# Kernel optimization log

Hardware: AMD Instinct MI355X
Metric: run time of the kernel (lower is better)

The kernel has to match this reference:

```python
import jax, jax.numpy as jnp
import numpy as np

N_EMBD = 256; N_HEAD = 16; CTX = 2048
V_HD = 32; KV_RANK = 32; Q_RANK = 96
ROPE_HD = 64; NOPE_HD = 32; HEAD_D = ROPE_HD + NOPE_HD  # 96
N_KEEP = CTX // 4  # 512
C_CURV = 1.0
EPS = 1e-6
B, T = 2, 2048


def rmsnorm(x, w):
    return x * jax.lax.rsqrt(jnp.mean(x * x, axis=-1, keepdims=True) + EPS) * w


def logmap(x, u, c):
    # log map from hyperbolic point x toward u (Poincare ball, curvature c)
    xn = jnp.linalg.norm(x, axis=-1, keepdims=True)
    sf = 2.0 / (1.0 + c * xn ** 2)                      # scaling_factor(x, c)
    mx = -x
    un = jnp.linalg.norm(u, axis=-1, keepdims=True)
    ip = jnp.sum(mx * u, axis=-1, keepdims=True)
    num = (1 + 2 * c * ip + c * un ** 2) * mx + (1 - c * xn ** 2) * u
    den = 1 + 2 * c * ip + (c ** 2) * (xn ** 2) * (un ** 2)
    mob = num / den                                      # mobius_addition(-x, u, c)
    an = jnp.linalg.norm(mob, axis=-1, keepdims=True)
    cf = 2.0 / (sf * (c ** 0.5))
    arg = jnp.clip(jnp.sqrt(c) * jnp.sqrt(an), -0.999, 0.999)
    return cf * jnp.arctanh(arg) * (mob / an)


def rope_apply(x, cos_seq, sin_seq):
    # x: [B,H,T,D]; cos/sin: [T,D//2] -> broadcast [1,1,T,D//2]
    c = cos_seq[None, None]; s = sin_seq[None, None]
    xr, xi = jnp.split(x, 2, axis=-1)
    return jnp.concatenate([xr * c - xi * s, xr * s + xi * c], axis=-1)


def attn(q, k, v, causal):
    d = q.shape[-1]
    s = jnp.einsum('bhqd,bhkd->bhqk', q, k) / jnp.sqrt(jnp.asarray(d, q.dtype))
    if causal:
        mask = jnp.tril(jnp.ones((s.shape[-2], s.shape[-1]), bool))
        s = jnp.where(mask, s, -jnp.inf)
    p = jax.nn.softmax(s, axis=-1)
    return jnp.einsum('bhqk,bhkd->bhqd', p, v)


def setup_inputs() -> dict:
    key = jax.random.key(0)
    ks = jax.random.split(key, 20)
    w = lambda k, shp: (jax.random.normal(k, shp, jnp.float32) * 0.02)
    NOPE_DIM = N_HEAD * NOPE_HD   # 512
    ROPE_DIM = N_HEAD * ROPE_HD   # 1024
    VAL_DIM = N_HEAD * V_HD       # 512
    # precompute_freqs_cis(rope_head_dim, ctx_len)
    freqs = 1.0 / (10000.0 ** (np.arange(0, ROPE_HD, 2, dtype=np.float32) / ROPE_HD))
    t = np.arange(CTX, dtype=np.float32)
    ang = np.outer(t, freqs)
    return {
        'x': jax.random.normal(ks[0], (B, T, N_EMBD), jnp.float32),
        'W_cq': w(ks[1], (N_EMBD, Q_RANK)),
        'q_norm_w': jnp.ones((Q_RANK,), jnp.float32),
        'W_dqn': w(ks[2], (Q_RANK, NOPE_DIM)),
        'W_dqr': w(ks[3], (Q_RANK, ROPE_DIM)),
        'W_ckv': w(ks[4], (N_EMBD, KV_RANK)),
        'kv_norm_w': jnp.ones((KV_RANK,), jnp.float32),
        'W_dkn': w(ks[5], (KV_RANK, NOPE_DIM)),
        'W_dv': w(ks[6], (KV_RANK, VAL_DIM)),
        'W_kr': w(ks[7], (N_EMBD, ROPE_HD)),
        'W_imp': w(ks[8], (N_EMBD, 1)),
        'b_imp': jnp.zeros((1,), jnp.float32),
        'W_selk': w(ks[9], (N_EMBD, N_HEAD * HEAD_D)),
        'W_selv': w(ks[10], (N_EMBD, VAL_DIM)),
        'W_wink': w(ks[11], (N_EMBD, N_HEAD * HEAD_D)),
        'W_winv': w(ks[12], (N_EMBD, VAL_DIM)),
        'W_gate': w(ks[13], (N_EMBD, 3)),
        'b_gate': jnp.zeros((3,), jnp.float32),
        'W_proj': w(ks[14], (N_HEAD * V_HD, N_EMBD)),
        'cos_f': jnp.asarray(np.cos(ang)),
        'sin_f': jnp.asarray(np.sin(ang)),
    }


def reference(x, W_cq, q_norm_w, W_dqn, W_dqr, W_ckv, kv_norm_w, W_dkn, W_dv, W_kr,
              W_imp, b_imp, W_selk, W_selv, W_wink, W_winv, W_gate, b_gate, W_proj,
              cos_f, sin_f):
    Bx, Tx, C = x.shape
    ref = jnp.pad(x[:, :-1, :], ((0, 0), (1, 0), (0, 0)))   # calculate_reference_point
    xh = logmap(ref, x, C_CURV)
    # compressed query path
    nq = rmsnorm(xh @ W_cq, q_norm_w)
    qn = (nq @ W_dqn).reshape(Bx, Tx, N_HEAD, NOPE_HD).transpose(0, 2, 1, 3)
    qr = (nq @ W_dqr).reshape(Bx, Tx, N_HEAD, ROPE_HD).transpose(0, 2, 1, 3)
    qr = rope_apply(qr, cos_f[:Tx], sin_f[:Tx])
    q = jnp.concatenate([qn, qr], axis=-1)                  # [B,H,T,96]
    # branch gate
    bw = jax.nn.softmax(jnp.mean(x @ W_gate + b_gate, axis=1), axis=-1)  # [B,3]
    # compressed KV path
    nkv = rmsnorm(x @ W_ckv, kv_norm_w)
    kn = (nkv @ W_dkn).reshape(Bx, Tx, N_HEAD, NOPE_HD).transpose(0, 2, 1, 3)
    v = (nkv @ W_dv).reshape(Bx, Tx, N_HEAD, V_HD).transpose(0, 2, 1, 3)
    kr = rope_apply((x @ W_kr)[:, None], cos_f[:Tx], sin_f[:Tx])  # [B,1,T,64]
    kr = jnp.broadcast_to(kr, (Bx, N_HEAD, Tx, ROPE_HD))
    k = jnp.concatenate([kn, kr], axis=-1)
    out_cmp = attn(q, k, v, causal=True)
    # token-selection branch (top-k important tokens, sorted)
    scores = (x @ W_imp + b_imp)[..., 0]                    # [B,T]
    _, idx = jax.lax.top_k(scores, min(N_KEEP, Tx))
    idx = jnp.sort(idx, axis=1)
    sel = jnp.take_along_axis(x, idx[:, :, None], axis=1)   # [B,K,C]
    sk = (sel @ W_selk).reshape(Bx, -1, N_HEAD, HEAD_D).transpose(0, 2, 1, 3)
    sv = (sel @ W_selv).reshape(Bx, -1, N_HEAD, V_HD).transpose(0, 2, 1, 3)
    out_sel = attn(q, sk, sv, causal=False)
    # sliding-window branch (training path -> full sequence, causal)
    wk = (x @ W_wink).reshape(Bx, Tx, N_HEAD, HEAD_D).transpose(0, 2, 1, 3)
    wv = (x @ W_winv).reshape(Bx, Tx, N_HEAD, V_HD).transpose(0, 2, 1, 3)
    out_win = attn(q, wk, wv, causal=True)
    w3 = bw[:, :, None, None, None]
    out = w3[:, 0] * out_cmp + w3[:, 1] * out_sel + w3[:, 2] * out_win
    out = out.transpose(0, 2, 1, 3).reshape(Bx, Tx, N_HEAD * V_HD)
    return out @ W_proj
```

## Files before the change

kernel.cpp:

```cpp
#include <hip/hip_runtime.h>
#include <hip/hip_bf16.h>
#include <math.h>

#define TT 2048
#define NE 256
#define NHEAD 16

typedef __attribute__((ext_vector_type(8))) short bf16x8;
typedef __attribute__((ext_vector_type(4))) float f32x4;
typedef __attribute__((ext_vector_type(16))) float f32x16;
typedef unsigned short ushort;
typedef __attribute__((ext_vector_type(8))) unsigned short us8;

__device__ __forceinline__ short f2bf(float x) {
  __hip_bfloat16 h = __float2bfloat16(x);
  return *reinterpret_cast<short*>(&h);
}
__device__ __forceinline__ float bf2f(ushort u) {
  unsigned v = ((unsigned)u) << 16;
  return __uint_as_float(v);
}

__global__ __launch_bounds__(256) void logmap_kernel(const float* __restrict__ x,
                                                     ushort* __restrict__ xhb,
                                                     ushort* __restrict__ xbf) {
  __shared__ float red[16];
  int row = blockIdx.x, tid = threadIdx.x;
  int t = row & (TT - 1);
  float uv = x[row * NE + tid];
  float rv = (t == 0) ? 0.f : x[row * NE - NE + tid];
  xbf[row * NE + tid] = (ushort)f2bf(uv);
  float a = rv * rv, bq = uv * uv, c2 = -rv * uv;
#pragma unroll
  for (int off = 32; off > 0; off >>= 1) {
    a += __shfl_down(a, off, 64);
    bq += __shfl_down(bq, off, 64);
    c2 += __shfl_down(c2, off, 64);
  }
  if ((tid & 63) == 0) {
    int w = tid >> 6;
    red[w] = a; red[4 + w] = bq; red[8 + w] = c2;
  }
  __syncthreads();
  float xn2 = red[0] + red[1] + red[2] + red[3];
  float un2 = red[4] + red[5] + red[6] + red[7];
  float ip  = red[8] + red[9] + red[10] + red[11];
  float den = 1.f + 2.f * ip + xn2 * un2;
  float mob = ((1.f + 2.f * ip + un2) * (-rv) + (1.f - xn2) * uv) / den;
  float m2 = mob * mob;
#pragma unroll
  for (int off = 32; off > 0; off >>= 1) m2 += __shfl_down(m2, off, 64);
  if ((tid & 63) == 0) red[12 + (tid >> 6)] = m2;
  __syncthreads();
  float an2 = red[12] + red[13] + red[14] + red[15];
  float an = sqrtf(an2);
  float cf = 1.f + xn2;
  float arg = fminf(sqrtf(an), 0.999f);
  xhb[row * NE + tid] = (ushort)f2bf(cf * atanhf(arg) * mob / an);
}

__global__ __launch_bounds__(256) void wtconv_all_kernel(
    const float* __restrict__ W_dqn, const float* __restrict__ W_dqr,
    const float* __restrict__ W_dkn, const float* __restrict__ W_dv,
    const float* __restrict__ W_selk, const float* __restrict__ W_selv,
    const float* __restrict__ W_wink, const float* __restrict__ W_winv,
    const float* __restrict__ W_proj, const float* __restrict__ W_cq,
    const float* __restrict__ W_ckv, const float* __restrict__ W_kr,
    const float* __restrict__ W_gate, const float* __restrict__ W_imp,
    ushort* __restrict__ Wt_q, ushort* __restrict__ Wt_kv,
    ushort* __restrict__ Wt_sel, ushort* __restrict__ Wt_win,
    ushort* __restrict__ Wt_proj, ushort* __restrict__ Wt_cq,
    ushort* __restrict__ Wt_nkv) {
  int i = blockIdx.x * 256 + threadIdx.x;
  const float scale = 0.147244458176154f;
  if (i < 147456) {
    int k = i / 1536, n = i - k * 1536;
    float v = (n < 512) ? W_dqn[(size_t)k * 512 + n] : W_dqr[(size_t)k * 1024 + (n - 512)];
    Wt_q[(size_t)n * 96 + k] = (ushort)f2bf(v * scale);
  } else if (i < 180224) {
    int j = i - 147456;
    int k = j >> 10, n = j & 1023;
    float v = (n < 512) ? W_dkn[(size_t)k * 512 + n] : W_dv[(size_t)k * 512 + (n - 512)];
    Wt_kv[(size_t)n * 32 + k] = (ushort)f2bf(v);
  } else if (i < 704512) {
    int j = i - 180224;
    int k = j >> 11, n = j & 2047;
    float v = (n < 1536) ? W_selk[(size_t)k * 1536 + n] : W_selv[(size_t)k * 512 + (n - 1536)];
    Wt_sel[(size_t)n * 256 + k] = (ushort)f2bf(v);
  } else if (i < 1228800) {
    int j = i - 704512;
    int k = j >> 11, n = j & 2047;
    float v = (n < 1536) ? W_wink[(size_t)k * 1536 + n] : W_winv[(size_t)k * 512 + (n - 1536)];
    Wt_win[(size_t)n * 256 + k] = (ushort)f2bf(v);
  } else if (i < 1359872) {
    int j = i - 1228800;
    int k = j >> 8, n = j & 255;
    Wt_proj[(size_t)n * 512 + k] = (ushort)f2bf(W_proj[(size_t)k * 256 + n]);
  } else if (i < 1392640) {
    int j = i - 1359872;
    int k = j >> 7, n = j & 127;
    float v = (n < 96) ? W_cq[(size_t)k * 96 + n] : 0.f;
    Wt_cq[(size_t)n * 256 + k] = (ushort)f2bf(v);
  } else if (i < 1425408) {
    int j = i - 1392640;
    int k = j >> 7, n = j & 127;
    float v;
    if (n < 32) v = W_ckv[(size_t)k * 32 + n];
    else if (n < 96) v = W_kr[(size_t)k * 64 + (n - 32)];
    else if (n < 99) v = W_gate[(size_t)k * 3 + (n - 96)];
    else if (n == 99) v = W_imp[k];
    else v = 0.f;
    Wt_nkv[(size_t)n * 256 + k] = (ushort)f2bf(v);
  }
}

__global__ __launch_bounds__(256) void gemm_kernel(const ushort* __restrict__ A,
                                                   const ushort* __restrict__ Bt,
                                                   void* __restrict__ Out,
                                                   const ushort* __restrict__ A2,
                                                   const ushort* __restrict__ Bt2,
                                                   void* __restrict__ Out2,
                                                   const int* __restrict__ selidx,
                                                   const float* __restrict__ cosp,
                                                   const float* __restrict__ sinp,
                                                   int K, int ldo, int obf16, int ropemode) {
  __shared__ __align__(16) short As[128 * 40];
  __shared__ __align__(16) short Bs[128 * 40];
  if (blockIdx.z == 1) { A = A2; Bt = Bt2; Out = Out2; }
  int m0 = blockIdx.x * 128, n0 = blockIdx.y * 128;
  int tid = threadIdx.x;
  int wv = tid >> 6, lane = tid & 63;
  int l15 = lane & 15, quad = lane >> 4;
  int wm = wv >> 1, wn = wv & 1;

  int r = tid >> 1, seg = tid & 1;
  int arow = m0 + r;
  if (selidx) arow = ((arow >> 9) * TT) + selidx[m0 + r];
  const ushort* ga = A + (size_t)arow * K + seg * 16;
  const ushort* gb = Bt + (size_t)(n0 + r) * K + seg * 16;

  f32x4 acc[4][4];
#pragma unroll
  for (int i = 0; i < 4; ++i)
#pragma unroll
    for (int j = 0; j < 4; ++j) acc[i][j] = (f32x4){0.f, 0.f, 0.f, 0.f};

  int nk = K >> 5;
  us8 apre0 = *(const us8*)ga, apre1 = *(const us8*)(ga + 8);
  us8 bpre0 = *(const us8*)gb, bpre1 = *(const us8*)(gb + 8);
  for (int kk = 0; kk < nk; ++kk) {
    __syncthreads();
    *(us8*)(As + r * 40 + seg * 16) = apre0;
    *(us8*)(As + r * 40 + seg * 16 + 8) = apre1;
    *(us8*)(Bs + r * 40 + seg * 16) = bpre0;
    *(us8*)(Bs + r * 40 + seg * 16 + 8) = bpre1;
    __syncthreads();
    if (kk + 1 < nk) {
      apre0 = *(const us8*)(ga + (kk + 1) * 32);
      apre1 = *(const us8*)(ga + (kk + 1) * 32 + 8);
      bpre0 = *(const us8*)(gb + (kk + 1) * 32);
      bpre1 = *(const us8*)(gb + (kk + 1) * 32 + 8);
    }
    bf16x8 af[4], bf[4];
#pragma unroll
    for (int mf = 0; mf < 4; ++mf)
      af[mf] = *(const bf16x8*)(As + (wm * 64 + mf * 16 + l15) * 40 + quad * 8);
#pragma unroll
    for (int nf = 0; nf < 4; ++nf)
      bf[nf] = *(const bf16x8*)(Bs + (wn * 64 + nf * 16 + l15) * 40 + quad * 8);
#pragma unroll
    for (int mf = 0; mf < 4; ++mf)
#pragma unroll
      for (int nf = 0; nf < 4; ++nf)
        acc[mf][nf] = __builtin_amdgcn_mfma_f32_16x16x32_bf16(af[mf], bf[nf], acc[mf][nf], 0, 0, 0);
  }

  if (ropemode && blockIdx.y >= 4) {
#pragma unroll
    for (int mf = 0; mf < 4; ++mf) {
#pragma unroll
      for (int nf = 0; nf < 2; ++nf) {
        int dd = nf * 16 + l15;
#pragma unroll
        for (int reg = 0; reg < 4; ++reg) {
          int row = m0 + wm * 64 + mf * 16 + quad * 4 + reg;
          int t = row & (TT - 1);
          float c = cosp[t * 32 + dd], s = sinp[t * 32 + dd];
          float xr = acc[mf][nf][reg], xi = acc[mf][nf + 2][reg];
          int col = n0 + wn * 64 + nf * 16 + l15;
          size_t oi = (size_t)row * ldo + col;
          ((ushort*)Out)[oi] = (ushort)f2bf(xr * c - xi * s);
          ((ushort*)Out)[oi + 32] = (ushort)f2bf(xr * s + xi * c);
        }
      }
    }
    return;
  }
#pragma unroll
  for (int mf = 0; mf < 4; ++mf) {
#pragma unroll
    for (int nf = 0; nf < 4; ++nf) {
#pragma unroll
      for (int reg = 0; reg < 4; ++reg) {
        int row = m0 + wm * 64 + mf * 16 + quad * 4 + reg;
        int col = n0 + wn * 64 + nf * 16 + l15;
        size_t oi = (size_t)row * ldo + col;
        float v = acc[mf][nf][reg];
        if (obf16) ((ushort*)Out)[oi] = (ushort)f2bf(v);
        else ((float*)Out)[oi] = v;
      }
    }
  }
}

__global__ __launch_bounds__(128) void norm_kernel(const float* __restrict__ nkvraw,
                                                   const float* __restrict__ nqraw,
                                                   const float* __restrict__ x,
                                                   const float* __restrict__ W_imp,
                                                   const float* __restrict__ b_imp,
                                                   const float* __restrict__ kvnw,
                                                   const float* __restrict__ qnw,
                                                   const float* __restrict__ cos_t,
                                                   const float* __restrict__ sin_t,
                                                   ushort* __restrict__ nkvb,
                                                   ushort* __restrict__ krbf,
                                                   float* __restrict__ scores,
                                                   ushort* __restrict__ nqb) {
  int tid = threadIdx.x;
  if (blockIdx.x < 4096) {
    int row = blockIdx.x;
    int t = row & (TT - 1);
    if (tid < 32) {
      float v = nkvraw[(size_t)row * 128 + tid];
      float ss = v * v;
#pragma unroll
      for (int off = 16; off > 0; off >>= 1) ss += __shfl_xor(ss, off, 32);
      nkvb[(size_t)row * 32 + tid] = (ushort)f2bf(v * rsqrtf(ss / 32.f + 1e-6f) * kvnw[tid]);
    } else if (tid < 64) {
      int dd = tid - 32;
      float xr = nkvraw[(size_t)row * 128 + 32 + dd];
      float xi = nkvraw[(size_t)row * 128 + 64 + dd];
      float c = cos_t[t * 32 + dd], s = sin_t[t * 32 + dd];
      krbf[(size_t)row * 64 + dd] = (ushort)f2bf(xr * c - xi * s);
      krbf[(size_t)row * 64 + dd + 32] = (ushort)f2bf(xr * s + xi * c);
    } else {
      int lane = tid - 64;
      float p = 0.f;
#pragma unroll
      for (int k = 0; k < 4; ++k) p += x[(size_t)row * 256 + lane + k * 64] * W_imp[lane + k * 64];
#pragma unroll
      for (int off = 32; off > 0; off >>= 1) p += __shfl_down(p, off, 64);
      if (lane == 0) scores[row] = p + b_imp[0];
    }
  } else {
    int row = blockIdx.x - 4096;
    __shared__ float red2[2];
    float v = (tid < 96) ? nqraw[(size_t)row * 128 + tid] : 0.f;
    float p = v * v;
#pragma unroll
    for (int off = 32; off > 0; off >>= 1) p += __shfl_down(p, off, 64);
    if ((tid & 63) == 0) red2[tid >> 6] = p;
    __syncthreads();
    float ss = red2[0] + red2[1];
    float sc = rsqrtf(ss / 96.f + 1e-6f);
    if (tid < 96) nqb[(size_t)row * 96 + tid] = (ushort)f2bf(v * sc * qnw[tid]);
  }
}

__global__ __launch_bounds__(256) void gate_kernel(const float* __restrict__ nkvraw,
                                                   const float* __restrict__ b_gate,
                                                   float* __restrict__ bw) {
  int tid = threadIdx.x;
  float a0 = 0, a1 = 0, a2 = 0, a3 = 0, a4 = 0, a5 = 0;
  for (int r = tid; r < 2 * TT; r += 256) {
    float g0 = nkvraw[(size_t)r * 128 + 96];
    float g1 = nkvraw[(size_t)r * 128 + 97];
    float g2 = nkvraw[(size_t)r * 128 + 98];
    if (r < TT) { a0 += g0; a1 += g1; a2 += g2; }
    else { a3 += g0; a4 += g1; a5 += g2; }
  }
  __shared__ float red[6][256];
  red[0][tid] = a0; red[1][tid] = a1; red[2][tid] = a2;
  red[3][tid] = a3; red[4][tid] = a4; red[5][tid] = a5;
  __syncthreads();
  for (int s = 128; s > 0; s >>= 1) {
    if (tid < s) {
#pragma unroll
      for (int q = 0; q < 6; ++q) red[q][tid] += red[q][tid + s];
    }
    __syncthreads();
  }
  if (tid == 0) {
    for (int b = 0; b < 2; ++b) {
      float v[3];
      float mx = -INFINITY;
      for (int j = 0; j < 3; ++j) {
        v[j] = red[b * 3 + j][0] / (float)TT + b_gate[j];
        mx = fmaxf(mx, v[j]);
      }
      float sum = 0.f;
      for (int j = 0; j < 3; ++j) { v[j] = expf(v[j] - mx); sum += v[j]; }
      for (int j = 0; j < 3; ++j) bw[b * 3 + j] = v[j] / sum;
    }
  }
}

__global__ __launch_bounds__(1024) void topk_rank_kernel(const float* __restrict__ scores,
                                                         int* __restrict__ flags) {
  int b = blockIdx.y, blk = blockIdx.x;
  int tid = threadIdx.x;
  __shared__ unsigned sk[TT];
#pragma unroll
  for (int e = 0; e < 2; ++e) {
    int i = tid + e * 1024;
    float s = scores[b * TT + i];
    unsigned u = __float_as_uint(s);
    u = (u & 0x80000000u) ? ~u : (u | 0x80000000u);
    sk[i] = u;
  }
  __syncthreads();
  int e = blk * 64 + (tid >> 4);
  int sub = tid & 15;
  unsigned u = sk[e];
  int r = 0;
  int j0 = sub * 128;
#pragma unroll 8
  for (int j = j0; j < j0 + 128; ++j) {
    unsigned v = sk[j];
    r += (int)((v > u) || (v == u && j < e));
  }
#pragma unroll
  for (int off = 8; off > 0; off >>= 1) r += __shfl_down(r, off, 16);
  if (sub == 0) flags[b * TT + e] = (r < 512) ? 1 : 0;
}

__global__ __launch_bounds__(1024) void topk_scan_kernel(const int* __restrict__ flags,
                                                         int* __restrict__ selidx) {
  int b = blockIdx.x, tid = threadIdx.x;
  __shared__ int pre[TT];
  int f0 = flags[b * TT + tid], f1 = flags[b * TT + tid + 1024];
  pre[tid] = f0;
  pre[tid + 1024] = f1;
  __syncthreads();
  for (int off = 1; off < TT; off <<= 1) {
    int a0 = (tid >= off) ? pre[tid - off] : 0;
    int a1 = (tid + 1024 >= off) ? pre[tid + 1024 - off] : 0;
    __syncthreads();
    pre[tid] += a0;
    pre[tid + 1024] += a1;
    __syncthreads();
  }
  if (f0) selidx[b * 512 + pre[tid] - 1] = tid;
  if (f1) selidx[b * 512 + pre[tid + 1024] - 1] = tid + 1024;
}

__global__ __launch_bounds__(512, 4) void flash_fused_kernel(
    const ushort* __restrict__ qbf,
    const ushort* __restrict__ kv,
    const ushort* __restrict__ krbf,
    const ushort* __restrict__ selt,
    const ushort* __restrict__ wint,
    const float* __restrict__ bw,
    ushort* __restrict__ attout) {
  __shared__ __align__(16) short smem[13312 + 4608 + 256];
  short* Ksm = smem;
  short* Vtm = smem + 13312;
  float* Ls  = (float*)(smem + 17920);

  int bx = blockIdx.x;
  int j = bx >> 5;
  int qtile = (j < 8) ? (15 - 2 * j) : (2 * (j - 8));
  int bh = bx & 31;
  int b = bh >> 4, h = bh & 15;
  int tid = threadIdx.x;
  int wv = tid >> 6;
  int qsub = wv >> 1;
  int khalf = wv & 1;
  int lane = tid & 63;
  int l31 = lane & 31, half = lane >> 5;

  int qrow0 = qtile * 128;
  for (int i = tid; i < 128 * 24; i += 512) {
    int qi = i / 24, dp = (i - qi * 24) * 4;
    int col = (dp < 32) ? (h * 32 + dp) : (512 + h * 64 + (dp - 32));
    *(ushort4*)(Ksm + qi * 104 + dp) =
        *(const ushort4*)(qbf + (size_t)(b * TT + qrow0 + qi) * 1536 + col);
  }
  __syncthreads();
  bf16x8 qf[6];
#pragma unroll
  for (int ks = 0; ks < 6; ++ks)
    qf[ks] = *(const bf16x8*)(Ksm + (qsub * 32 + l31) * 104 + ks * 16 + half * 8);
  __syncthreads();

  short* kdst[3];
#pragma unroll
  for (int c = 0; c < 3; ++c) {
    int i = c * 512 + tid;
    int kj = i / 24, dp = (i - kj * 24) * 4;
    kdst[c] = &Ksm[kj * 104 + dp];
  }
  int vd0 = (tid & 15) * 2, vkjp = (tid >> 4) * 2;
  short* vdsta = &Vtm[(vd0 + 0) * 72 + vkjp];
  short* vdstb = &Vtm[(vd0 + 1) * 72 + vkjp];

  f32x16 oacc;
#pragma unroll
  for (int r2 = 0; r2 < 16; ++r2) oacc[r2] = 0.f;

#define PREFETCH(KP, VA, VB)                                  \
  {                                                           \
    _Pragma("unroll") for (int c = 0; c < 3; ++c) {           \
      KP[c] = *(const ushort4*)ksrc[c];                       \
      ksrc[c] += kstep[c];                                    \
    }                                                         \
    VA = *(const ushort2*)vsrcA;                              \
    VB = *(const ushort2*)vsrcB;                              \
    vsrcA += vstep;                                           \
    vsrcB += vstep;                                           \
  }

#define COMMIT(KP, VA, VB, SL)                                           \
  {                                                                      \
    _Pragma("unroll") for (int c = 0; c < 3; ++c)                        \
      *(ushort4*)(kdst[c] + (SL) * (64 * 104)) = KP[c];                  \
    *(unsigned*)(vdsta + (SL) * (32 * 72)) =                             \
        (unsigned)VA.x | ((unsigned)VB.x << 16);                         \
    *(unsigned*)(vdstb + (SL) * (32 * 72)) =                             \
        (unsigned)VA.y | ((unsigned)VB.y << 16);                         \
  }

  for (int s = 0; s < 3; ++s) {
    const ushort *kb1, *kb2, *vb;
    size_t krs1, krs2, vrs;
    int split, Tk, causal;
    if (s == 0) {
      kb1 = kv + h * 32;        krs1 = 1024; split = 32;
      kb2 = krbf;               krs2 = 64;
      vb = kv + 512 + h * 32;   vrs = 1024;
      Tk = TT; causal = 1;
    } else if (s == 1) {
      kb1 = selt + h * 96;      krs1 = 2048; split = 96;
      kb2 = selt;               krs2 = 2048;
      vb = selt + 1536 + h * 32; vrs = 2048;
      Tk = 512; causal = 0;
    } else {
      kb1 = wint + h * 96;      krs1 = 2048; split = 96;
      kb2 = wint;               krs2 = 2048;
      vb = wint + 1536 + h * 32; vrs = 2048;
      Tk = TT; causal = 1;
    }
    size_t bTk = (size_t)b * Tk;

    const ushort* ksrc[3];
    int kstep[3];
#pragma unroll
    for (int c = 0; c < 3; ++c) {
      int i = c * 512 + tid;
      int kj = i / 24, dp = (i - kj * 24) * 4;
      if (dp < split) { ksrc[c] = kb1 + (bTk + kj) * krs1 + dp; kstep[c] = (int)(64 * krs1); }
      else            { ksrc[c] = kb2 + (bTk + kj) * krs2 + (dp - split); kstep[c] = (int)(64 * krs2); }
    }
    const ushort* vsrcA = vb + (bTk + vkjp) * vrs + vd0;
    const ushort* vsrcB = vb + (bTk + vkjp + 1) * vrs + vd0;
    int vstep = (int)(64 * vrs);

    ushort4 kpre0[3], kpre1[3];
    ushort2 vpa0, vpb0, vpa1, vpb1;

    f32x16 of;
#pragma unroll
    for (int r2 = 0; r2 < 16; ++r2) of[r2] = 0.f;
    float lsum = 0.f;

    auto do_tile = [&](int kt, const short* Kss, const short* Vss) {
      int krow0 = kt * 64;
      f32x16 sfT[2];
#pragma unroll
      for (int r2 = 0; r2 < 16; ++r2) { sfT[0][r2] = 0.f; sfT[1][r2] = 0.f; }
#pragma unroll
      for (int ks = 0; ks < 6; ++ks) {
#pragma unroll
        for (int kb = 0; kb < 2; ++kb) {
          bf16x8 ak = *(const bf16x8*)(Kss + (kb * 32 + l31) * 104 + ks * 16 + half * 8);
          sfT[kb] = __builtin_amdgcn_mfma_f32_32x32x16_bf16(ak, qf[ks], sfT[kb], 0, 0, 0);
        }
      }
      int qg = qrow0 + qsub * 32 + l31;
      int domask = causal && (kt >= 2 * qtile);
      unsigned w01[2][4], w23[2][4];
#pragma unroll
      for (int kb = 0; kb < 2; ++kb) {
#pragma unroll
        for (int gg = 0; gg < 4; ++gg) {
          int key0 = krow0 + kb * 32 + 8 * gg + 4 * half;
          float t0 = sfT[kb][gg * 4 + 0];
          float t1 = sfT[kb][gg * 4 + 1];
          float t2 = sfT[kb][gg * 4 + 2];
          float t3 = sfT[kb][gg * 4 + 3];
          if (domask) {
            if (key0 + 0 > qg) t0 = -INFINITY;
            if (key0 + 1 > qg) t1 = -INFINITY;
            if (key0 + 2 > qg) t2 = -INFINITY;
            if (key0 + 3 > qg) t3 = -INFINITY;
          }
          float p0 = __builtin_amdgcn_exp2f(fminf(t0, 43.3f));
          float p1 = __builtin_amdgcn_exp2f(fminf(t1, 43.3f));
          float p2 = __builtin_amdgcn_exp2f(fminf(t2, 43.3f));
          float p3 = __builtin_amdgcn_exp2f(fminf(t3, 43.3f));
          lsum += (p0 + p1) + (p2 + p3);
          asm("v_cvt_pk_bf16_f32 %0, %1, %2" : "=v"(w01[kb][gg]) : "v"(p0), "v"(p1));
          asm("v_cvt_pk_bf16_f32 %0, %1, %2" : "=v"(w23[kb][gg]) : "v"(p2), "v"(p3));
        }
      }
#pragma unroll
      for (int ks2 = 0; ks2 < 4; ++ks2) {
        int kb = ks2 >> 1, gA = 2 * (ks2 & 1);
        unsigned a0 = w01[kb][gA], b0 = w01[kb][gA + 1];
        unsigned a1 = w23[kb][gA], b1 = w23[kb][gA + 1];
        asm("v_permlane32_swap_b32 %0, %1" : "+v"(a0), "+v"(b0));
        asm("v_permlane32_swap_b32 %0, %1" : "+v"(a1), "+v"(b1));
        union { unsigned u[4]; bf16x8 v; } ap;
        ap.u[0] = a0; ap.u[1] = a1; ap.u[2] = b0; ap.u[3] = b1;
        bf16x8 bv = *(const bf16x8*)(Vss + l31 * 72 + ks2 * 16 + half * 8);
        of = __builtin_amdgcn_mfma_f32_32x32x16_bf16(ap.v, bv, of, 0, 0, 0);
      }
    };

    int nkt = causal ? (2 * qtile + 2) : 8;
    PREFETCH(kpre0, vpa0, vpb0);
    PREFETCH(kpre1, vpa1, vpb1);
    for (int kt = 0; kt < nkt; kt += 2) {
      __syncthreads();
      COMMIT(kpre0, vpa0, vpb0, 0);
      COMMIT(kpre1, vpa1, vpb1, 1);
      if (kt + 2 < nkt) PREFETCH(kpre0, vpa0, vpb0);
      if (kt + 3 < nkt) PREFETCH(kpre1, vpa1, vpb1);
      __syncthreads();
      if (khalf == 0) do_tile(kt, Ksm, Vtm);
      else            do_tile(kt + 1, Ksm + 64 * 104, Vtm + 32 * 72);
    }

    lsum += __shfl_xor(lsum, 32, 64);
    __syncthreads();
    float* red = (float*)Ksm;
    int rbase = (qsub * 64 + lane) * 17;
    if (khalf == 1) {
#pragma unroll
      for (int r2 = 0; r2 < 16; ++r2) red[rbase + r2] = of[r2];
      red[rbase + 16] = lsum;
    }
    __syncthreads();
    if (khalf == 0) {
#pragma unroll
      for (int r2 = 0; r2 < 16; ++r2) of[r2] += red[rbase + r2];
      lsum += red[rbase + 16];
      if (half == 0) Ls[qsub * 32 + l31] = lsum;
    }
    asm volatile("s_waitcnt lgkmcnt(0)" ::: "memory");
    if (khalf == 0) {
      float wgt = bw[b * 3 + s];
#pragma unroll
      for (int reg = 0; reg < 16; ++reg) {
        int ql = (reg & 3) + 8 * (reg >> 2) + 4 * half;
        oacc[reg] += of[reg] * (wgt / Ls[qsub * 32 + ql]);
      }
    }
  }
#undef PREFETCH
#undef COMMIT

  if (khalf == 0) {
#pragma unroll
    for (int reg = 0; reg < 16; ++reg) {
      int trow = qrow0 + qsub * 32 + (reg & 3) + 8 * (reg >> 2) + 4 * half;
      attout[(size_t)(b * TT + trow) * 512 + h * 32 + l31] = (ushort)f2bf(oacc[reg]);
    }
  }
}

extern "C" void kernel_launch(void* const* d_in, const int* in_sizes, int n_in,
                              void* d_out, int out_size, void* d_ws, size_t ws_size,
                              hipStream_t stream) {
  const float* x      = (const float*)d_in[0];
  const float* W_cq   = (const float*)d_in[1];
  const float* qnw    = (const float*)d_in[2];
  const float* W_dqn  = (const float*)d_in[3];
  const float* W_dqr  = (const float*)d_in[4];
  const float* W_ckv  = (const float*)d_in[5];
  const float* kvnw   = (const float*)d_in[6];
  const float* W_dkn  = (const float*)d_in[7];
  const float* W_dv   = (const float*)d_in[8];
  const float* W_kr   = (const float*)d_in[9];
  const float* W_imp  = (const float*)d_in[10];
  const float* b_imp  = (const float*)d_in[11];
  const float* W_selk = (const float*)d_in[12];
  const float* W_selv = (const float*)d_in[13];
  const float* W_wink = (const float*)d_in[14];
  const float* W_winv = (const float*)d_in[15];
  const float* W_gate = (const float*)d_in[16];
  const float* b_gate = (const float*)d_in[17];
  const float* W_proj = (const float*)d_in[18];
  const float* cos_f  = (const float*)d_in[19];
  const float* sin_f  = (const float*)d_in[20];
  float* out = (float*)d_out;
  float* ws  = (float*)d_ws;

  size_t off = 0;
  auto alloc = [&](size_t n) {
    float* p = ws + off;
    off += (n + 255) & ~(size_t)255;
    return p;
  };
  const int ROWS = 2 * TT;
  ushort* xbf     = (ushort*)alloc((size_t)ROWS * 128);
  ushort* xhb     = (ushort*)alloc((size_t)ROWS * 128);
  float* nqraw    = alloc((size_t)ROWS * 128);
  float* nkvraw   = alloc((size_t)ROWS * 128);
  ushort* nqb     = (ushort*)alloc((size_t)ROWS * 48);
  ushort* qbf     = (ushort*)alloc((size_t)ROWS * 768);
  ushort* nkvb    = (ushort*)alloc((size_t)ROWS * 16);
  ushort* kvtmp   = (ushort*)alloc((size_t)ROWS * 512);
  ushort* krbf    = (ushort*)alloc((size_t)ROWS * 32);
  float* scores   = alloc(ROWS);
  float* bwp      = alloc(8);
  int* selidx     = (int*)alloc(1024);
  int* selflags   = (int*)alloc(ROWS);
  ushort* seltmp  = (ushort*)alloc((size_t)1024 * 1024);
  ushort* wintmp  = (ushort*)alloc((size_t)ROWS * 1024);
  ushort* attoutb = (ushort*)alloc((size_t)ROWS * 256);
  ushort* Wt_q    = (ushort*)alloc((size_t)1536 * 48);
  ushort* Wt_kv   = (ushort*)alloc((size_t)1024 * 16);
  ushort* Wt_sel  = (ushort*)alloc((size_t)2048 * 128);
  ushort* Wt_win  = (ushort*)alloc((size_t)2048 * 128);
  ushort* Wt_proj = (ushort*)alloc((size_t)256 * 256);
  ushort* Wt_cq   = (ushort*)alloc((size_t)128 * 128);
  ushort* Wt_nkv  = (ushort*)alloc((size_t)128 * 128);

  wtconv_all_kernel<<<5568, 256, 0, stream>>>(
      W_dqn, W_dqr, W_dkn, W_dv, W_selk, W_selv, W_wink, W_winv, W_proj,
      W_cq, W_ckv, W_kr, W_gate, W_imp,
      Wt_q, Wt_kv, Wt_sel, Wt_win, Wt_proj, Wt_cq, Wt_nkv);

  logmap_kernel<<<ROWS, 256, 0, stream>>>(x, xhb, xbf);

  gemm_kernel<<<dim3(32, 1, 2), 256, 0, stream>>>(xhb, Wt_cq, nqraw, xbf, Wt_nkv, nkvraw,
                                                  nullptr, nullptr, nullptr, 256, 128, 0, 0);
  norm_kernel<<<2 * ROWS, 128, 0, stream>>>(nkvraw, nqraw, x, W_imp, b_imp, kvnw, qnw,
                                            cos_f, sin_f, nkvb, krbf, scores, nqb);
  gemm_kernel<<<dim3(32, 12), 256, 0, stream>>>(nqb, Wt_q, qbf, nullptr, nullptr, nullptr,
                                                nullptr, cos_f, sin_f, 96, 1536, 1, 1);
  gemm_kernel<<<dim3(32, 8), 256, 0, stream>>>(nkvb, Wt_kv, kvtmp, nullptr, nullptr, nullptr,
                                               nullptr, nullptr, nullptr, 32, 1024, 1, 0);
  gate_kernel<<<1, 256, 0, stream>>>(nkvraw, b_gate, bwp);
  topk_rank_kernel<<<dim3(32, 2), 1024, 0, stream>>>(scores, selflags);
  topk_scan_kernel<<<2, 1024, 0, stream>>>(selflags, selidx);
  gemm_kernel<<<dim3(8, 16), 256, 0, stream>>>(xbf, Wt_sel, seltmp, nullptr, nullptr, nullptr,
                                               selidx, nullptr, nullptr, 256, 2048, 1, 0);
  gemm_kernel<<<dim3(32, 16), 256, 0, stream>>>(xbf, Wt_win, wintmp, nullptr, nullptr, nullptr,
                                                nullptr, nullptr, nullptr, 256, 2048, 1, 0);

  flash_fused_kernel<<<512, 512, 0, stream>>>(qbf, kvtmp, krbf, seltmp, wintmp, bwp, attoutb);

  gemm_kernel<<<dim3(32, 2), 256, 0, stream>>>(attoutb, Wt_proj, out, nullptr, nullptr, nullptr,
                                               nullptr, nullptr, nullptr, 512, 256, 0, 0);
}
```

Measured before the change: 299.5 us.

## Merge launches: fuse logmap into weight prep, batch GEMMs, fold gate into GEMM epilogue

Merges the logmap and weight-conversion kernels into one prep kernel, and batches independent GEMMs (q/kv projections, window/selection projections) into single launches through a z-dimension with per-slice parameters. The gate reduction moves into the first GEMM's epilogue via atomics, and the gate softmax is computed inside the flash kernel. The top-k scan is rewritten with a wave-shuffle prefix sum, and flash launch bounds change from 4 to 2. The intent is to cut launch overhead and serial small kernels, at the cost of atomics, early-return blocks in the batched GEMMs, and a different occupancy hint for flash.

```diff
diff --git a/kernel.cpp b/kernel.cpp
--- a/kernel.cpp
+++ b/kernel.cpp
@@ -21,45 +21,8 @@
   return __uint_as_float(v);
 }
 
-__global__ __launch_bounds__(256) void logmap_kernel(const float* __restrict__ x,
-                                                     ushort* __restrict__ xhb,
-                                                     ushort* __restrict__ xbf) {
-  __shared__ float red[16];
-  int row = blockIdx.x, tid = threadIdx.x;
-  int t = row & (TT - 1);
-  float uv = x[row * NE + tid];
-  float rv = (t == 0) ? 0.f : x[row * NE - NE + tid];
-  xbf[row * NE + tid] = (ushort)f2bf(uv);
-  float a = rv * rv, bq = uv * uv, c2 = -rv * uv;
-#pragma unroll
-  for (int off = 32; off > 0; off >>= 1) {
-    a += __shfl_down(a, off, 64);
-    bq += __shfl_down(bq, off, 64);
-    c2 += __shfl_down(c2, off, 64);
-  }
-  if ((tid & 63) == 0) {
-    int w = tid >> 6;
-    red[w] = a; red[4 + w] = bq; red[8 + w] = c2;
-  }
-  __syncthreads();
-  float xn2 = red[0] + red[1] + red[2] + red[3];
-  float un2 = red[4] + red[5] + red[6] + red[7];
-  float ip  = red[8] + red[9] + red[10] + red[11];
-  float den = 1.f + 2.f * ip + xn2 * un2;
-  float mob = ((1.f + 2.f * ip + un2) * (-rv) + (1.f - xn2) * uv) / den;
-  float m2 = mob * mob;
-#pragma unroll
-  for (int off = 32; off > 0; off >>= 1) m2 += __shfl_down(m2, off, 64);
-  if ((tid & 63) == 0) red[12 + (tid >> 6)] = m2;
-  __syncthreads();
-  float an2 = red[12] + red[13] + red[14] + red[15];
-  float an = sqrtf(an2);
-  float cf = 1.f + xn2;
-  float arg = fminf(sqrtf(an), 0.999f);
-  xhb[row * NE + tid] = (ushort)f2bf(cf * atanhf(arg) * mob / an);
-}
-
-__global__ __launch_bounds__(256) void wtconv_all_kernel(
+__global__ __launch_bounds__(256) void prep_kernel(
+    const float* __restrict__ x, ushort* __restrict__ xhb, ushort* __restrict__ xbf,
     const float* __restrict__ W_dqn, const float* __restrict__ W_dqr,
     const float* __restrict__ W_dkn, const float* __restrict__ W_dv,
     const float* __restrict__ W_selk, const float* __restrict__ W_selv,
@@ -70,8 +33,45 @@
     ushort* __restrict__ Wt_q, ushort* __restrict__ Wt_kv,
     ushort* __restrict__ Wt_sel, ushort* __restrict__ Wt_win,
     ushort* __restrict__ Wt_proj, ushort* __restrict__ Wt_cq,
-    ushort* __restrict__ Wt_nkv) {
-  int i = blockIdx.x * 256 + threadIdx.x;
+    ushort* __restrict__ Wt_nkv, float* __restrict__ gacc) {
+  __shared__ float red[16];
+  int bx = blockIdx.x, tid = threadIdx.x;
+  if (bx < 4096) {
+    int row = bx;
+    int t = row & (TT - 1);
+    float uv = x[row * NE + tid];
+    float rv = (t == 0) ? 0.f : x[row * NE - NE + tid];
+    xbf[row * NE + tid] = (ushort)f2bf(uv);
+    float a = rv * rv, bq = uv * uv, c2 = -rv * uv;
+#pragma unroll
+    for (int off = 32; off > 0; off >>= 1) {
+      a += __shfl_down(a, off, 64);
+      bq += __shfl_down(bq, off, 64);
+      c2 += __shfl_down(c2, off, 64);
+    }
+    if ((tid & 63) == 0) {
+      int w = tid >> 6;
+      red[w] = a; red[4 + w] = bq; red[8 + w] = c2;
+    }
+    __syncthreads();
+    float xn2 = red[0] + red[1] + red[2] + red[3];
+    float un2 = red[4] + red[5] + red[6] + red[7];
+    float ip  = red[8] + red[9] + red[10] + red[11];
+    float den = 1.f + 2.f * ip + xn2 * un2;
+    float mob = ((1.f + 2.f * ip + un2) * (-rv) + (1.f - xn2) * uv) / den;
+    float m2 = mob * mob;
+#pragma unroll
+    for (int off = 32; off > 0; off >>= 1) m2 += __shfl_down(m2, off, 64);
+    if ((tid & 63) == 0) red[12 + (tid >> 6)] = m2;
+    __syncthreads();
+    float an2 = red[12] + red[13] + red[14] + red[15];
+    float an = sqrtf(an2);
+    float cf = 1.f + xn2;
+    float arg = fminf(sqrtf(an), 0.999f);
+    xhb[row * NE + tid] = (ushort)f2bf(cf * atanhf(arg) * mob / an);
+    return;
+  }
+  int i = (bx - 4096) * 256 + tid;
   const float scale = 0.147244458176154f;
   if (i < 147456) {
     int k = i / 1536, n = i - k * 1536;
@@ -111,6 +111,8 @@
     else if (n == 99) v = W_imp[k];
     else v = 0.f;
     Wt_nkv[(size_t)n * 256 + k] = (ushort)f2bf(v);
+  } else if (i < 1425414) {
+    gacc[i - 1425408] = 0.f;
   }
 }
 
@@ -120,13 +122,21 @@
                                                    const ushort* __restrict__ A2,
                                                    const ushort* __restrict__ Bt2,
                                                    void* __restrict__ Out2,
-                                                   const int* __restrict__ selidx,
+                                                   const int* __restrict__ selidx2,
                                                    const float* __restrict__ cosp,
                                                    const float* __restrict__ sinp,
-                                                   int K, int ldo, int obf16, int ropemode) {
+                                                   float* __restrict__ gateacc,
+                                                   int K, int ldo, int obf16, int ropemode,
+                                                   int K2, int ldo2, int obf2, int rope2,
+                                                   int xlim2, int ylim2) {
   __shared__ __align__(16) short As[128 * 40];
   __shared__ __align__(16) short Bs[128 * 40];
-  if (blockIdx.z == 1) { A = A2; Bt = Bt2; Out = Out2; }
+  const int* selidx = nullptr;
+  if (blockIdx.z == 1) {
+    if ((int)blockIdx.x >= xlim2 || (int)blockIdx.y >= ylim2) return;
+    A = A2; Bt = Bt2; Out = Out2; selidx = selidx2;
+    K = K2; ldo = ldo2; obf16 = obf2; ropemode = rope2;
+  }
   int m0 = blockIdx.x * 128, n0 = blockIdx.y * 128;
   int tid = threadIdx.x;
   int wv = tid >> 6, lane = tid & 63;
@@ -210,6 +220,14 @@
         else ((float*)Out)[oi] = v;
       }
     }
+  }
+  if (gateacc != nullptr && blockIdx.z == 1 && wn == 1 && l15 < 3) {
+    float ssum = 0.f;
+#pragma unroll
+    for (int mf = 0; mf < 4; ++mf)
+#pragma unroll
+      for (int reg = 0; reg < 4; ++reg) ssum += acc[mf][2][reg];
+    atomicAdd(&gateacc[(m0 >> 11) * 3 + l15], ssum);
   }
 }
 
@@ -267,44 +285,6 @@
   }
 }
 
-__global__ __launch_bounds__(256) void gate_kernel(const float* __restrict__ nkvraw,
-                                                   const float* __restrict__ b_gate,
-                                                   float* __restrict__ bw) {
-  int tid = threadIdx.x;
-  float a0 = 0, a1 = 0, a2 = 0, a3 = 0, a4 = 0, a5 = 0;
-  for (int r = tid; r < 2 * TT; r += 256) {
-    float g0 = nkvraw[(size_t)r * 128 + 96];
-    float g1 = nkvraw[(size_t)r * 128 + 97];
-    float g2 = nkvraw[(size_t)r * 128 + 98];
-    if (r < TT) { a0 += g0; a1 += g1; a2 += g2; }
-    else { a3 += g0; a4 += g1; a5 += g2; }
-  }
-  __shared__ float red[6][256];
-  red[0][tid] = a0; red[1][tid] = a1; red[2][tid] = a2;
-  red[3][tid] = a3; red[4][tid] = a4; red[5][tid] = a5;
-  __syncthreads();
-  for (int s = 128; s > 0; s >>= 1) {
-    if (tid < s) {
-#pragma unroll
-      for (int q = 0; q < 6; ++q) red[q][tid] += red[q][tid + s];
-    }
-    __syncthreads();
-  }
-  if (tid == 0) {
-    for (int b = 0; b < 2; ++b) {
-      float v[3];
-      float mx = -INFINITY;
-      for (int j = 0; j < 3; ++j) {
-        v[j] = red[b * 3 + j][0] / (float)TT + b_gate[j];
-        mx = fmaxf(mx, v[j]);
-      }
-      float sum = 0.f;
-      for (int j = 0; j < 3; ++j) { v[j] = expf(v[j] - mx); sum += v[j]; }
-      for (int j = 0; j < 3; ++j) bw[b * 3 + j] = v[j] / sum;
-    }
-  }
-}
-
 __global__ __launch_bounds__(1024) void topk_rank_kernel(const float* __restrict__ scores,
                                                          int* __restrict__ flags) {
   int b = blockIdx.y, blk = blockIdx.x;
@@ -337,30 +317,34 @@
 __global__ __launch_bounds__(1024) void topk_scan_kernel(const int* __restrict__ flags,
                                                          int* __restrict__ selidx) {
   int b = blockIdx.x, tid = threadIdx.x;
-  __shared__ int pre[TT];
-  int f0 = flags[b * TT + tid], f1 = flags[b * TT + tid + 1024];
-  pre[tid] = f0;
-  pre[tid + 1024] = f1;
+  __shared__ int wsum[16];
+  int2 f = *(const int2*)(flags + b * TT + 2 * tid);
+  int local = f.x + f.y;
+  int lane = tid & 63, wv = tid >> 6;
+  int sc = local;
+#pragma unroll
+  for (int off = 1; off < 64; off <<= 1) {
+    int t = __shfl_up(sc, off, 64);
+    if (lane >= off) sc += t;
+  }
+  if (lane == 63) wsum[wv] = sc;
   __syncthreads();
-  for (int off = 1; off < TT; off <<= 1) {
-    int a0 = (tid >= off) ? pre[tid - off] : 0;
-    int a1 = (tid + 1024 >= off) ? pre[tid + 1024 - off] : 0;
-    __syncthreads();
-    pre[tid] += a0;
-    pre[tid + 1024] += a1;
-    __syncthreads();
-  }
-  if (f0) selidx[b * 512 + pre[tid] - 1] = tid;
-  if (f1) selidx[b * 512 + pre[tid + 1024] - 1] = tid + 1024;
-}
-
-__global__ __launch_bounds__(512, 4) void flash_fused_kernel(
+  int woff = 0;
+  for (int w = 0; w < wv; ++w) woff += wsum[w];
+  int p0 = woff + (sc - local) + f.x;
+  int p1 = p0 + f.y;
+  if (f.x) selidx[b * 512 + p0 - 1] = 2 * tid;
+  if (f.y) selidx[b * 512 + p1 - 1] = 2 * tid + 1;
+}
+
+__global__ __launch_bounds__(512, 2) void flash_fused_kernel(
     const ushort* __restrict__ qbf,
     const ushort* __restrict__ kv,
     const ushort* __restrict__ krbf,
     const ushort* __restrict__ selt,
     const ushort* __restrict__ wint,
-    const float* __restrict__ bw,
+    const float* __restrict__ gacc,
+    const float* __restrict__ b_gate,
     ushort* __restrict__ attout) {
   __shared__ __align__(16) short smem[13312 + 4608 + 256];
   short* Ksm = smem;
@@ -378,6 +362,17 @@
   int khalf = wv & 1;
   int lane = tid & 63;
   int l31 = lane & 31, half = lane >> 5;
+
+  float w0, w1, w2;
+  {
+    float g0 = gacc[b * 3 + 0] * (1.0f / 2048.0f) + b_gate[0];
+    float g1 = gacc[b * 3 + 1] * (1.0f / 2048.0f) + b_gate[1];
+    float g2 = gacc[b * 3 + 2] * (1.0f / 2048.0f) + b_gate[2];
+    float mx = fmaxf(g0, fmaxf(g1, g2));
+    float e0 = expf(g0 - mx), e1 = expf(g1 - mx), e2 = expf(g2 - mx);
+    float inv = 1.f / (e0 + e1 + e2);
+    w0 = e0 * inv; w1 = e1 * inv; w2 = e2 * inv;
+  }
 
   int qrow0 = qtile * 128;
   for (int i = tid; i < 128 * 24; i += 512) {
@@ -559,7 +554,7 @@
     }
     asm volatile("s_waitcnt lgkmcnt(0)" ::: "memory");
     if (khalf == 0) {
-      float wgt = bw[b * 3 + s];
+      float wgt = (s == 0) ? w0 : ((s == 1) ? w1 : w2);
 #pragma unroll
       for (int reg = 0; reg < 16; ++reg) {
         int ql = (reg & 3) + 8 * (reg >> 2) + 4 * half;
@@ -623,7 +618,7 @@
   ushort* kvtmp   = (ushort*)alloc((size_t)ROWS * 512);
   ushort* krbf    = (ushort*)alloc((size_t)ROWS * 32);
   float* scores   = alloc(ROWS);
-  float* bwp      = alloc(8);
+  float* gacc     = alloc(8);
   int* selidx     = (int*)alloc(1024);
   int* selflags   = (int*)alloc(ROWS);
   ushort* seltmp  = (ushort*)alloc((size_t)1024 * 1024);
@@ -637,31 +632,38 @@
   ushort* Wt_cq   = (ushort*)alloc((size_t)128 * 128);
   ushort* Wt_nkv  = (ushort*)alloc((size_t)128 * 128);
 
-  wtconv_all_kernel<<<5568, 256, 0, stream>>>(
+  prep_kernel<<<4096 + 5569, 256, 0, stream>>>(
+      x, xhb, xbf,
       W_dqn, W_dqr, W_dkn, W_dv, W_selk, W_selv, W_wink, W_winv, W_proj,
       W_cq, W_ckv, W_kr, W_gate, W_imp,
-      Wt_q, Wt_kv, Wt_sel, Wt_win, Wt_proj, Wt_cq, Wt_nkv);
-
-  logmap_kernel<<<ROWS, 256, 0, stream>>>(x, xhb, xbf);
-
-  gemm_kernel<<<dim3(32, 1, 2), 256, 0, stream>>>(xhb, Wt_cq, nqraw, xbf, Wt_nkv, nkvraw,
-                                                  nullptr, nullptr, nullptr, 256, 128, 0, 0);
+      Wt_q, Wt_kv, Wt_sel, Wt_win, Wt_proj, Wt_cq, Wt_nkv, gacc);
+
+  gemm_kernel<<<dim3(32, 1, 2), 256, 0, stream>>>(
+      xhb, Wt_cq, nqraw, xbf, Wt_nkv, nkvraw,
+      nullptr, nullptr, nullptr, gacc,
+      256, 128, 0, 0, 256, 128, 0, 0, 32, 1);
+
   norm_kernel<<<2 * ROWS, 128, 0, stream>>>(nkvraw, nqraw, x, W_imp, b_imp, kvnw, qnw,
                                             cos_f, sin_f, nkvb, krbf, scores, nqb);
-  gemm_kernel<<<dim3(32, 12), 256, 0, stream>>>(nqb, Wt_q, qbf, nullptr, nullptr, nullptr,
-                                                nullptr, cos_f, sin_f, 96, 1536, 1, 1);
-  gemm_kernel<<<dim3(32, 8), 256, 0, stream>>>(nkvb, Wt_kv, kvtmp, nullptr, nullptr, nullptr,
-                                               nullptr, nullptr, nullptr, 32, 1024, 1, 0);
-  gate_kernel<<<1, 256, 0, stream>>>(nkvraw, b_gate, bwp);
+
+  gemm_kernel<<<dim3(32, 12, 2), 256, 0, stream>>>(
+      nqb, Wt_q, qbf, nkvb, Wt_kv, kvtmp,
+      nullptr, cos_f, sin_f, nullptr,
+      96, 1536, 1, 1, 32, 1024, 1, 0, 32, 8);
+
   topk_rank_kernel<<<dim3(32, 2), 1024, 0, stream>>>(scores, selflags);
   topk_scan_kernel<<<2, 1024, 0, stream>>>(selflags, selidx);
-  gemm_kernel<<<dim3(8, 16), 256, 0, stream>>>(xbf, Wt_sel, seltmp, nullptr, nullptr, nullptr,
-                                               selidx, nullptr, nullptr, 256, 2048, 1, 0);
-  gemm_kernel<<<dim3(32, 16), 256, 0, stream>>>(xbf, Wt_win, wintmp, nullptr, nullptr, nullptr,
-                                                nullptr, nullptr, nullptr, 256, 2048, 1, 0);
-
-  flash_fused_kernel<<<512, 512, 0, stream>>>(qbf, kvtmp, krbf, seltmp, wintmp, bwp, attoutb);
-
-  gemm_kernel<<<dim3(32, 2), 256, 0, stream>>>(attoutb, Wt_proj, out, nullptr, nullptr, nullptr,
-                                               nullptr, nullptr, nullptr, 512, 256, 0, 0);
-}
+
+  gemm_kernel<<<dim3(32, 16, 2), 256, 0, stream>>>(
+      xbf, Wt_win, wintmp, xbf, Wt_sel, seltmp,
+      selidx, nullptr, nullptr, nullptr,
+      256, 2048, 1, 0, 256, 2048, 1, 0, 8, 16);
+
+  flash_fused_kernel<<<512, 512, 0, stream>>>(qbf, kvtmp, krbf, seltmp, wintmp,
+                                              gacc, b_gate, attoutb);
+
+  gemm_kernel<<<dim3(32, 2, 1), 256, 0, stream>>>(
+      attoutb, Wt_proj, out, nullptr, nullptr, nullptr,
+      nullptr, nullptr, nullptr, nullptr,
+      512, 256, 0, 0, 0, 0, 0, 0, 0, 0);
+}
```

After: 311.0 us. +3.9%, slower.
